# Kernel optimization log

Hardware: AMD Instinct MI355X
Metric: run time of the kernel (lower is better)

## Reference

```python
import jax, jax.numpy as jnp
import numpy as np

D_MODEL = 1024
N_HEADS = 16
FACTOR = 2
KEY_DIM = D_MODEL // N_HEADS            # 64
HEAD_DIM = D_MODEL * FACTOR // N_HEADS  # 128
SCALING = KEY_DIM ** -0.5
BSZ, SEQ = 2, 2048


def _rel_pos(slen):
    # angle: 1/10000**linspace(0,1,key_dim//2), each value repeated twice
    half = jnp.asarray(1.0) / jnp.power(10000.0, jnp.linspace(0.0, 1.0, KEY_DIM // 2))
    angle = jnp.repeat(half, 2)                              # [key_dim]
    decay = jnp.log(1.0 - 2.0 ** (-5.0 - jnp.arange(N_HEADS, dtype=jnp.float32)))  # [h], negative
    idx = jnp.arange(slen, dtype=jnp.float32)
    sin = jnp.sin(idx[:, None] * angle[None, :])             # [s, key_dim]
    cos = jnp.cos(idx[:, None] * angle[None, :])
    diff = idx[:, None] - idx[None, :]                       # [s, s]
    tril = diff >= 0
    mask = jnp.where(tril[None], jnp.exp(diff[None] * decay[:, None, None]), 0.0)  # [h, s, s]
    mask = mask / jnp.sqrt(mask.sum(axis=-1, keepdims=True))
    return sin, cos, mask


def _rotate_every_two(x):
    x1 = x[..., ::2]
    x2 = x[..., 1::2]
    return jnp.stack((-x2, x1), axis=-1).reshape(x.shape)


def _theta_shift(x, sin, cos):
    return x * cos + _rotate_every_two(x) * sin


def setup_inputs() -> dict:
    key = jax.random.key(0)
    ks = jax.random.split(key, 11)
    s = 1.0 / np.sqrt(D_MODEL)
    s2 = 1.0 / np.sqrt(D_MODEL * FACTOR)
    return {
        "x": jax.random.normal(ks[0], (BSZ, SEQ, D_MODEL), jnp.float32),
        "q_w": jax.random.uniform(ks[1], (D_MODEL, D_MODEL), jnp.float32, -s, s),
        "q_b": jax.random.uniform(ks[2], (D_MODEL,), jnp.float32, -s, s),
        "k_w": jax.random.uniform(ks[3], (D_MODEL, D_MODEL), jnp.float32, -s, s),
        "k_b": jax.random.uniform(ks[4], (D_MODEL,), jnp.float32, -s, s),
        "v_w": jax.random.uniform(ks[5], (D_MODEL, D_MODEL * FACTOR), jnp.float32, -s, s),
        "v_b": jax.random.uniform(ks[6], (D_MODEL * FACTOR,), jnp.float32, -s, s),
        "g_w": jax.random.uniform(ks[7], (D_MODEL, D_MODEL * FACTOR), jnp.float32, -s, s),
        "g_b": jax.random.uniform(ks[8], (D_MODEL * FACTOR,), jnp.float32, -s, s),
        "o_w": jax.random.uniform(ks[9], (D_MODEL * FACTOR, D_MODEL), jnp.float32, -s2, s2),
        "o_b": jax.random.uniform(ks[10], (D_MODEL,), jnp.float32, -s2, s2),
    }


def _forward(x, q_w, q_b, k_w, k_b, v_w, v_b, g_w, g_b, o_w, o_b):
    bsz, slen, _ = x.shape
    sin, cos, mask = _rel_pos(slen)
    q = x @ q_w + q_b
    k = (x @ k_w + k_b) * SCALING
    v = x @ v_w + v_b
    g = x @ g_w + g_b
    # [b, h, s, key_dim]
    q = q.reshape(bsz, slen, N_HEADS, KEY_DIM).transpose(0, 2, 1, 3)
    k = k.reshape(bsz, slen, N_HEADS, KEY_DIM).transpose(0, 2, 1, 3)
    qr = _theta_shift(q, sin, cos)
    kr = _theta_shift(k, sin, cos)
    vr = v.reshape(bsz, slen, N_HEADS, HEAD_DIM).transpose(0, 2, 1, 3)  # [b,h,s,head_dim]
    qk = jnp.einsum('bhmd,bhnd->bhmn', qr, kr) * mask                  # decay-masked scores
    denom = jnp.clip(jnp.abs(jax.lax.stop_gradient(qk).sum(axis=-1, keepdims=True)), 1.0, None)
    qk = qk / denom
    out = jnp.einsum('bhmn,bhnd->bhmd', qk, vr).transpose(0, 2, 1, 3)  # [b,s,h,head_dim]
    # per-head LayerNorm over head_dim, no affine
    mu = out.mean(axis=-1, keepdims=True)
    var = out.var(axis=-1, keepdims=True)
    out = (out - mu) / jnp.sqrt(var + 1e-5)
    out = out.reshape(bsz, slen, N_HEADS * HEAD_DIM)
    out = jax.nn.silu(g) * out
    return out @ o_w + o_b


def reference(x, q_w, q_b, k_w, k_b, v_w, v_b, g_w, g_b, o_w, o_b):
    return _forward(x, q_w, q_b, k_w, k_b, v_w, v_b, g_w, g_b, o_w, o_b)
```

## Files before the change

### kernel.cpp

```cpp
#include <hip/hip_runtime.h>
#include <hip/hip_bf16.h>


typedef __hip_bfloat16 bf16;
typedef short bf16x4 __attribute__((ext_vector_type(4)));
typedef short bf16x8 __attribute__((ext_vector_type(8)));
typedef float floatx4 __attribute__((ext_vector_type(4)));

#define B_SZ 2
#define SEQ 2048
#define NH 16
#define KD 64
#define HD 128

#define ASYNC16(gp, lp)                                                             \
  __builtin_amdgcn_global_load_lds(                                                 \
      (const __attribute__((address_space(1))) unsigned int*)(unsigned long long)(const void*)(gp), \
      (__attribute__((address_space(3))) unsigned int*)(unsigned int)(unsigned long long)(void*)(lp), \
      16, 0, 0)

__device__ __forceinline__ float b2f(bf16 x) { return __bfloat162float(x); }
__device__ __forceinline__ bf16 f2b(float x) { return __float2bfloat16(x); }

#define MFMA16(a, bb, c) __builtin_amdgcn_mfma_f32_16x16x32_bf16(a, bb, c, 0, 0, 0)

__global__ void convert_k(const float* __restrict__ in, bf16* __restrict__ out) {
  int i = blockIdx.x * 256 + threadIdx.x;
  float4 v = reinterpret_cast<const float4*>(in)[i];
  union { bf16 h[4]; bf16x4 v4; } u;
  u.h[0] = f2b(v.x); u.h[1] = f2b(v.y); u.h[2] = f2b(v.z); u.h[3] = f2b(v.w);
  reinterpret_cast<bf16x4*>(out)[i] = u.v4;
}

__global__ void transpose_k(const float* __restrict__ in, bf16* __restrict__ out,
                            int K, int N) {
  __shared__ float tile[32][33];
  int tx = threadIdx.x, ty = threadIdx.y;
  int n0 = blockIdx.x * 32, k0 = blockIdx.y * 32;
#pragma unroll
  for (int j = 0; j < 4; ++j)
    tile[ty + j * 8][tx] = in[(size_t)(k0 + ty + j * 8) * N + n0 + tx];
  __syncthreads();
#pragma unroll
  for (int j = 0; j < 4; ++j)
    out[(size_t)(n0 + ty + j * 8) * K + k0 + tx] = f2b(tile[tx][ty + j * 8]);
}

template <int BM, int BN, int KDIM, int MODE>
__global__ __launch_bounds__(256, 2) void gemm_bt(
    const bf16* __restrict__ A, const bf16* __restrict__ Bt, int Ndim,
    const float* __restrict__ bias_q, const float* __restrict__ bias_k,
    const float* __restrict__ bias_v, const float* __restrict__ bias_g,
    float* __restrict__ outCqk, bf16* __restrict__ out_v,
    float* __restrict__ out_g, float* __restrict__ outF) {
  __shared__ bf16 As[BM * 32];
  __shared__ bf16 Bs[BN * 32];
  const int tid = threadIdx.x;
  const int wave = tid >> 6, lane = tid & 63;
  const int quad = lane >> 4, l16 = lane & 15;
  const int m0 = blockIdx.y * BM, n0 = blockIdx.x * BN;
  constexpr int FI = BM / 32;
  constexpr int FJ = BN / 32;
  const int wm = (wave >> 1) * (BM / 2), wn = (wave & 1) * (BN / 2);

  floatx4 acc[FI][FJ] = {};

  for (int k0 = 0; k0 < KDIM; k0 += 32) {
#pragma unroll
    for (int j = 0; j < BM / 64; ++j) {
      int cbase = (j * 4 + wave) * 64;
      int c = cbase + lane;
      const bf16* g = A + (size_t)(m0 + (c >> 2)) * KDIM + k0 + (c & 3) * 8;
      ASYNC16(g, &As[cbase * 8]);
    }
#pragma unroll
    for (int j = 0; j < BN / 64; ++j) {
      int cbase = (j * 4 + wave) * 64;
      int c = cbase + lane;
      const bf16* g = Bt + (size_t)(n0 + (c >> 2)) * KDIM + k0 + (c & 3) * 8;
      ASYNC16(g, &Bs[cbase * 8]);
    }
    __syncthreads();

    bf16x8 af[FI], bfr[FJ];
#pragma unroll
    for (int i = 0; i < FI; ++i)
      af[i] = *(const bf16x8*)&As[(wm + i * 16 + l16) * 32 + quad * 8];
#pragma unroll
    for (int j = 0; j < FJ; ++j)
      bfr[j] = *(const bf16x8*)&Bs[(wn + j * 16 + l16) * 32 + quad * 8];
#pragma unroll
    for (int i = 0; i < FI; ++i)
#pragma unroll
      for (int j = 0; j < FJ; ++j)
        acc[i][j] = MFMA16(af[i], bfr[j], acc[i][j]);
    __syncthreads();
  }

#pragma unroll
  for (int i = 0; i < FI; ++i) {
#pragma unroll
    for (int j = 0; j < FJ; ++j) {
      int gn = n0 + wn + j * 16 + l16;
      if (MODE == 0 && gn >= 2048 && gn < 4096) {
        int jj = gn - 2048;
        int s0 = m0 + wm + i * 16 + quad * 4;
        union { bf16 e[4]; unsigned long long u8; } pk;
#pragma unroll
        for (int r = 0; r < 4; ++r) pk.e[r] = f2b(acc[i][j][r] + bias_v[jj]);
        int b2 = s0 >> 11, srel = s0 & 2047;
        int h2 = jj >> 7, dloc = jj & 127;
        size_t bh2 = (size_t)b2 * NH + h2;
        size_t idx = ((bh2 * 64 + (srel >> 5)) * 8 + (dloc >> 4)) * 512 +
                     (size_t)(((srel >> 3) & 3) * 16 + (dloc & 15)) * 8 +
                     (srel & 7);
        *(unsigned long long*)&out_v[idx] = pk.u8;
      } else {
#pragma unroll
        for (int r = 0; r < 4; ++r) {
          int gm = m0 + wm + i * 16 + quad * 4 + r;
          float v = acc[i][j][r];
          if (MODE == 1) {
            v += bias_q[gn];
            outF[(size_t)gm * Ndim + gn] = v;
          } else {
            if (gn < 2048) {
              bool is_k = gn >= 1024;
              int jj = is_k ? gn - 1024 : gn;
              v += is_k ? bias_k[jj] : bias_q[jj];
              if (is_k) v *= 0.125f;
              outCqk[(size_t)gm * 2048 + gn] = v;
            } else {
              int jj = gn - 4096;
              v += bias_g[jj];
              out_g[(size_t)gm * 2048 + jj] = v;
            }
          }
        }
      }
    }
  }
}

__global__ void router_k(const float* __restrict__ Cqk,
                         bf16* __restrict__ qh, bf16* __restrict__ ql,
                         bf16* __restrict__ kh, bf16* __restrict__ kl) {
  int t = blockIdx.x * 256 + threadIdx.x;
  int row = t >> 10, pc = t & 1023;
  int b = row >> 11, s = row & 2047;
  bool is_k = pc >= 512;
  int jj = (pc - (is_k ? 512 : 0)) * 2;
  int h = jj >> 6, d = jj & 63, ii = d >> 1;
  float2 v = *(const float2*)&Cqk[(size_t)row * 2048 + pc * 2];
  float half = exp2f(-(float)ii * (13.287712379549449f / 31.0f));
  float ang = (float)s * half;
  float sn = sinf(ang), cs = cosf(ang);
  float e = v.x * cs - v.y * sn;
  float o = v.y * cs + v.x * sn;
  bf16 eh = f2b(e), oh = f2b(o);
  bf16 el = f2b(e - b2f(eh)), ol = f2b(o - b2f(oh));
  size_t idx = (((size_t)b * NH + h) * SEQ + s) * KD + d;
  bf16* ph = is_k ? kh : qh;
  bf16* pl = is_k ? kl : ql;
  union { bf16 h2[2]; unsigned u; } uh, ul;
  uh.h2[0] = eh; uh.h2[1] = oh;
  ul.h2[0] = el; ul.h2[1] = ol;
  *(unsigned*)&ph[idx] = uh.u;
  *(unsigned*)&pl[idx] = ul.u;
}

__global__ __launch_bounds__(256, 4) void retention_k(
    const bf16* __restrict__ qh, const bf16* __restrict__ ql,
    const bf16* __restrict__ kh, const bf16* __restrict__ kl,
    const bf16* __restrict__ vf, const float* __restrict__ g,
    bf16* __restrict__ gated) {
  __shared__ bf16 KHs[2][32 * 64];
  __shared__ bf16 KLs[2][32 * 64];
  const int tid = threadIdx.x;
  const int wave = tid >> 6, lane = tid & 63;
  const int quad = lane >> 4, l16 = lane & 15;
  const int bid = blockIdx.x;
  const int grp_raw = bid & 31;
  const int bh = bid >> 5;
  const int h = bh & 15, b = bh >> 4;
  const int grp = ((bh >> 3) & 1) ? (31 - grp_raw) : grp_raw;
  const int st = grp * 4 + wave;
  const int m0 = st * 16;
  const int ntiles = 2 * grp + 2;

  const float t = exp2f(-(float)(5 + h));
  const float lng = log1pf(-t);
  const float log2g = lng * 1.44269504088896340736f;

  float rf;
  {
    int m = m0 + l16;
    rf = exp2f((float)m * log2g) *
         rsqrtf(-expm1f((float)(m + 1) * lng) / t);
  }
  const float gstep = exp2f(-32.0f * log2g);
  float cfq[8];
#pragma unroll
  for (int i = 0; i < 8; ++i) {
    int hh = i >> 2, r = i & 3;
    cfq[i] = exp2f(-(float)(hh * 16 + quad * 4 + r) * log2g);
  }

  const size_t qoff = ((size_t)bh * SEQ + m0 + l16) * KD;
  bf16x8 aq0h = *(const bf16x8*)&qh[qoff + quad * 8];
  bf16x8 aq1h = *(const bf16x8*)&qh[qoff + 32 + quad * 8];
  bf16x8 aq0l = *(const bf16x8*)&ql[qoff + quad * 8];
  bf16x8 aq1l = *(const bf16x8*)&ql[qoff + 32 + quad * 8];

  floatx4 oacc[8] = {};
  float rs = 0.f;

  const bf16* khb = kh + (size_t)bh * SEQ * KD;
  const bf16* klb = kl + (size_t)bh * SEQ * KD;
  const bf16* vfb = vf + (size_t)bh * 64 * 8 * 512;
  const int lo8 = lane * 8;

  auto stage = [&](int nt, int buf) {
    const int n0s = nt * 32;
#pragma unroll
    for (int j = 0; j < 2; ++j) {
      int cc = wave * 2 + j;
      const bf16* src = (cc < 4) ? khb : klb;
      bf16* dst = (cc < 4) ? KHs[buf] : KLs[buf];
      int r = ((cc & 3) * 8) + (lane >> 3);
      int s = lane & 7;
      int q = (s - r) & 7;
      ASYNC16(src + (size_t)(n0s + r) * KD + q * 8, &dst[(cc & 3) * 512]);
    }
  };

  auto buildPA = [&](const floatx4* sc, int n0) -> bf16x8 {
    const int m = m0 + l16;
    const bool full = (m0 >= n0 + 31);
    unsigned d[4];
#pragma unroll
    for (int hh = 0; hh < 2; ++hh) {
      float p[4];
#pragma unroll
      for (int r = 0; r < 4; ++r) {
        float pv;
        if (full) {
          pv = sc[hh][r] * rf * cfq[hh * 4 + r];
        } else {
          int n = n0 + hh * 16 + quad * 4 + r;
          pv = (m >= n) ? sc[hh][r] * rf * cfq[hh * 4 + r] : 0.f;
        }
        rs += pv;
        p[r] = pv;
      }
      union { bf16 hx[2]; unsigned u; } u0, u1;
      u0.hx[0] = f2b(p[0]); u0.hx[1] = f2b(p[1]);
      u1.hx[0] = f2b(p[2]); u1.hx[1] = f2b(p[3]);
      d[hh * 2 + 0] = u0.u;
      d[hh * 2 + 1] = u1.u;
    }
    unsigned a0 = d[0], b0 = d[2];
    asm("v_permlane32_swap_b32 %0, %1" : "+v"(a0), "+v"(b0));
    asm("v_permlane16_swap_b32 %0, %1" : "+v"(a0), "+v"(b0));
    unsigned a1 = d[1], b1 = d[3];
    asm("v_permlane32_swap_b32 %0, %1" : "+v"(a1), "+v"(b1));
    asm("v_permlane16_swap_b32 %0, %1" : "+v"(a1), "+v"(b1));
    union { unsigned u[4]; bf16x8 v; } pu;
    pu.u[0] = a0; pu.u[1] = a1; pu.u[2] = b0; pu.u[3] = b1;
    return pu.v;
  };

  stage(0, 0);
  for (int nt = 0; nt < ntiles; ++nt) {
    const int n0 = nt * 32;
    const int cur = nt & 1;
    asm volatile("s_waitcnt vmcnt(0) lgkmcnt(0)" ::: "memory");
    __syncthreads();

    const bool act = (n0 <= m0 + 15);

    bf16x8 vv[8];
    if (act) {
#pragma unroll
      for (int c = 0; c < 8; ++c)
        vv[c] = *(const bf16x8*)(vfb + ((size_t)nt * 8 + c) * 512 + lo8);
    }

    {
      int pf = (nt + 1 < ntiles) ? nt + 1 : nt;
      stage(pf, cur ^ 1);
    }

    if (act) {
      floatx4 sc[2];
#pragma unroll
      for (int hh = 0; hh < 2; ++hh) {
        int krow = hh * 16 + l16;
        int c0 = ((quad + krow) & 7) * 8;
        int c1 = ((quad + 4 + krow) & 7) * 8;
        bf16x8 bkh0 = *(const bf16x8*)&KHs[cur][krow * 64 + c0];
        bf16x8 bkh1 = *(const bf16x8*)&KHs[cur][krow * 64 + c1];
        bf16x8 bkl0 = *(const bf16x8*)&KLs[cur][krow * 64 + c0];
        bf16x8 bkl1 = *(const bf16x8*)&KLs[cur][krow * 64 + c1];
        floatx4 z1 = {0.f, 0.f, 0.f, 0.f}, z2 = z1, z3 = z1;
        z1 = MFMA16(bkh0, aq0h, z1);
        z2 = MFMA16(bkh0, aq0l, z2);
        z3 = MFMA16(bkl0, aq0h, z3);
        z1 = MFMA16(bkh1, aq1h, z1);
        z2 = MFMA16(bkh1, aq1l, z2);
        z3 = MFMA16(bkl1, aq1h, z3);
        sc[hh] = z1 + z2 + z3;
      }

      bf16x8 pa = buildPA(sc, n0);
      rf *= gstep;

#pragma unroll
      for (int dt = 0; dt < 8; ++dt)
        oacc[dt] = MFMA16(pa, vv[dt], oacc[dt]);
    }
  }

  {
    float v = rs;
    v += __shfl_xor(v, 16);
    v += __shfl_xor(v, 32);
    float inv_den[4];
#pragma unroll
    for (int r = 0; r < 4; ++r) {
      float dsum = __shfl(v, quad * 4 + r);
      inv_den[r] = 1.0f / fmaxf(fabsf(dsum), 1.0f);
    }
    float s1[4] = {}, s2[4] = {};
#pragma unroll
    for (int dt = 0; dt < 8; ++dt) {
#pragma unroll
      for (int r = 0; r < 4; ++r) {
        float vv2 = oacc[dt][r] * inv_den[r];
        oacc[dt][r] = vv2;
        s1[r] += vv2;
        s2[r] += vv2 * vv2;
      }
    }
    float mean[4], istd[4];
#pragma unroll
    for (int r = 0; r < 4; ++r) {
      float a = s1[r], q2 = s2[r];
      a += __shfl_xor(a, 1); a += __shfl_xor(a, 2);
      a += __shfl_xor(a, 4); a += __shfl_xor(a, 8);
      q2 += __shfl_xor(q2, 1); q2 += __shfl_xor(q2, 2);
      q2 += __shfl_xor(q2, 4); q2 += __shfl_xor(q2, 8);
      mean[r] = a * (1.0f / 128.0f);
      float var = q2 * (1.0f / 128.0f) - mean[r] * mean[r];
      istd[r] = rsqrtf(fmaxf(var, 0.0f) + 1e-5f);
    }
#pragma unroll
    for (int dt = 0; dt < 8; ++dt) {
#pragma unroll
      for (int r = 0; r < 4; ++r) {
        int m = m0 + quad * 4 + r;
        int col = h * HD + dt * 16 + l16;
        float vv2 = (oacc[dt][r] - mean[r]) * istd[r];
        float gv = g[((size_t)b * SEQ + m) * 2048 + col];
        float sg = gv / (1.0f + expf(-gv));
        gated[((size_t)b * SEQ + m) * 2048 + col] = f2b(sg * vv2);
      }
    }
  }
}

extern "C" void kernel_launch(void* const* d_in, const int* in_sizes, int n_in,
                              void* d_out, int out_size, void* d_ws,
                              size_t ws_size, hipStream_t stream) {
  const float* x   = (const float*)d_in[0];
  const float* q_w = (const float*)d_in[1];
  const float* q_b = (const float*)d_in[2];
  const float* k_w = (const float*)d_in[3];
  const float* k_b = (const float*)d_in[4];
  const float* v_w = (const float*)d_in[5];
  const float* v_b = (const float*)d_in[6];
  const float* g_w = (const float*)d_in[7];
  const float* g_b = (const float*)d_in[8];
  const float* o_w = (const float*)d_in[9];
  const float* o_b = (const float*)d_in[10];

  char* ws = (char*)d_ws;
  bf16* Wt    = (bf16*)ws; ws += (size_t)6144 * 1024 * 2;
  bf16* oT    = (bf16*)ws; ws += (size_t)1024 * 2048 * 2;
  bf16* xb    = (bf16*)ws; ws += (size_t)4096 * 1024 * 2;
  float* Cqk  = (float*)ws; ws += (size_t)4096 * 2048 * 4;
  bf16* qhb   = (bf16*)ws; ws += (size_t)32 * 2048 * 64 * 2;
  bf16* qlb   = (bf16*)ws; ws += (size_t)32 * 2048 * 64 * 2;
  bf16* khb   = (bf16*)ws; ws += (size_t)32 * 2048 * 64 * 2;
  bf16* klb   = (bf16*)ws; ws += (size_t)32 * 2048 * 64 * 2;
  bf16* vfb   = (bf16*)ws; ws += (size_t)32 * 64 * 8 * 512 * 2;
  float* gbuf = (float*)ws; ws += (size_t)2 * 2048 * 2048 * 4;
  bf16* gated = (bf16*)ws; ws += (size_t)4096 * 2048 * 2;

  convert_k<<<(4096 * 1024 / 4) / 256, 256, 0, stream>>>(x, xb);

  dim3 tb(32, 8);
  transpose_k<<<dim3(1024 / 32, 1024 / 32), tb, 0, stream>>>(q_w, Wt, 1024, 1024);
  transpose_k<<<dim3(1024 / 32, 1024 / 32), tb, 0, stream>>>(k_w, Wt + (size_t)1024 * 1024, 1024, 1024);
  transpose_k<<<dim3(2048 / 32, 1024 / 32), tb, 0, stream>>>(v_w, Wt + (size_t)2048 * 1024, 1024, 2048);
  transpose_k<<<dim3(2048 / 32, 1024 / 32), tb, 0, stream>>>(g_w, Wt + (size_t)4096 * 1024, 1024, 2048);
  transpose_k<<<dim3(1024 / 32, 2048 / 32), tb, 0, stream>>>(o_w, oT, 2048, 1024);

  gemm_bt<128, 128, 1024, 0><<<dim3(6144 / 128, 4096 / 128), 256, 0, stream>>>(
      xb, Wt, 6144, q_b, k_b, v_b, g_b, Cqk, vfb, gbuf, nullptr);

  router_k<<<(4096 * 1024) / 256, 256, 0, stream>>>(Cqk, qhb, qlb, khb, klb);

  retention_k<<<dim3(1024), 256, 0, stream>>>(
      qhb, qlb, khb, klb, vfb, gbuf, gated);

  gemm_bt<128, 64, 2048, 1><<<dim3(1024 / 64, 4096 / 128), 256, 0, stream>>>(
      gated, oT, 1024, o_b, nullptr, nullptr, nullptr, nullptr, nullptr,
      nullptr, (float*)d_out);
}
```

Before: 337.1 us.

## Fuse rotary theta-shift and hi/lo bf16 split into QKV GEMM epilogue

The separate router kernel is removed. The QKV projection GEMM epilogue now applies the bias, the K scaling, the rotary sin/cos rotation (taking the pair partner via a lane shuffle) and the hi/lo bf16 split, then writes q/k straight to the head-major buffers. This drops the large fp32 Cqk intermediate write and re-read and one kernel launch. In exchange the GEMM epilogue does per-element transcendental math and narrow 2-byte scattered stores, which may lengthen the epilogue and raise register pressure.

```diff
diff --git a/kernel.cpp b/kernel.cpp
--- a/kernel.cpp
+++ b/kernel.cpp
@@ -51,8 +51,10 @@
     const bf16* __restrict__ A, const bf16* __restrict__ Bt, int Ndim,
     const float* __restrict__ bias_q, const float* __restrict__ bias_k,
     const float* __restrict__ bias_v, const float* __restrict__ bias_g,
-    float* __restrict__ outCqk, bf16* __restrict__ out_v,
-    float* __restrict__ out_g, float* __restrict__ outF) {
+    bf16* __restrict__ qh, bf16* __restrict__ ql,
+    bf16* __restrict__ kh, bf16* __restrict__ kl,
+    bf16* __restrict__ out_v, float* __restrict__ out_g,
+    float* __restrict__ outF) {
   __shared__ bf16 As[BM * 32];
   __shared__ bf16 Bs[BN * 32];
   const int tid = threadIdx.x;
@@ -102,7 +104,32 @@
 #pragma unroll
     for (int j = 0; j < FJ; ++j) {
       int gn = n0 + wn + j * 16 + l16;
-      if (MODE == 0 && gn >= 2048 && gn < 4096) {
+      if (MODE == 0 && gn < 2048) {
+        bool is_k = gn >= 1024;
+        int jq = is_k ? gn - 1024 : gn;
+        int hd = jq >> 6, d = jq & 63;
+        float halfv = exp2f(-(float)(d >> 1) * (13.287712379549449f / 31.0f));
+        bf16* ph = is_k ? kh : qh;
+        bf16* pl = is_k ? kl : ql;
+        float bias = is_k ? bias_k[jq] : bias_q[jq];
+#pragma unroll
+        for (int r = 0; r < 4; ++r) {
+          int gm = m0 + wm + i * 16 + quad * 4 + r;
+          float v = acc[i][j][r] + bias;
+          if (is_k) v *= 0.125f;
+          int srel = gm & 2047, b2 = gm >> 11;
+          float ang = (float)srel * halfv;
+          float sn = sinf(ang), cs = cosf(ang);
+          float partner = __shfl_xor(v, 1);
+          float res = (gn & 1) ? (v * cs + partner * sn)
+                               : (v * cs - partner * sn);
+          bf16 rh = f2b(res);
+          bf16 rl = f2b(res - b2f(rh));
+          size_t idx = (((size_t)b2 * NH + hd) * SEQ + srel) * KD + d;
+          ph[idx] = rh;
+          pl[idx] = rl;
+        }
+      } else if (MODE == 0 && gn >= 2048 && gn < 4096) {
         int jj = gn - 2048;
         int s0 = m0 + wm + i * 16 + quad * 4;
         union { bf16 e[4]; unsigned long long u8; } pk;
@@ -124,49 +151,14 @@
             v += bias_q[gn];
             outF[(size_t)gm * Ndim + gn] = v;
           } else {
-            if (gn < 2048) {
-              bool is_k = gn >= 1024;
-              int jj = is_k ? gn - 1024 : gn;
-              v += is_k ? bias_k[jj] : bias_q[jj];
-              if (is_k) v *= 0.125f;
-              outCqk[(size_t)gm * 2048 + gn] = v;
-            } else {
-              int jj = gn - 4096;
-              v += bias_g[jj];
-              out_g[(size_t)gm * 2048 + jj] = v;
-            }
+            int jj = gn - 4096;
+            v += bias_g[jj];
+            out_g[(size_t)gm * 2048 + jj] = v;
           }
         }
       }
     }
   }
-}
-
-__global__ void router_k(const float* __restrict__ Cqk,
-                         bf16* __restrict__ qh, bf16* __restrict__ ql,
-                         bf16* __restrict__ kh, bf16* __restrict__ kl) {
-  int t = blockIdx.x * 256 + threadIdx.x;
-  int row = t >> 10, pc = t & 1023;
-  int b = row >> 11, s = row & 2047;
-  bool is_k = pc >= 512;
-  int jj = (pc - (is_k ? 512 : 0)) * 2;
-  int h = jj >> 6, d = jj & 63, ii = d >> 1;
-  float2 v = *(const float2*)&Cqk[(size_t)row * 2048 + pc * 2];
-  float half = exp2f(-(float)ii * (13.287712379549449f / 31.0f));
-  float ang = (float)s * half;
-  float sn = sinf(ang), cs = cosf(ang);
-  float e = v.x * cs - v.y * sn;
-  float o = v.y * cs + v.x * sn;
-  bf16 eh = f2b(e), oh = f2b(o);
-  bf16 el = f2b(e - b2f(eh)), ol = f2b(o - b2f(oh));
-  size_t idx = (((size_t)b * NH + h) * SEQ + s) * KD + d;
-  bf16* ph = is_k ? kh : qh;
-  bf16* pl = is_k ? kl : ql;
-  union { bf16 h2[2]; unsigned u; } uh, ul;
-  uh.h2[0] = eh; uh.h2[1] = oh;
-  ul.h2[0] = el; ul.h2[1] = ol;
-  *(unsigned*)&ph[idx] = uh.u;
-  *(unsigned*)&pl[idx] = ul.u;
 }
 
 __global__ __launch_bounds__(256, 4) void retention_k(
@@ -388,7 +380,6 @@
   bf16* Wt    = (bf16*)ws; ws += (size_t)6144 * 1024 * 2;
   bf16* oT    = (bf16*)ws; ws += (size_t)1024 * 2048 * 2;
   bf16* xb    = (bf16*)ws; ws += (size_t)4096 * 1024 * 2;
-  float* Cqk  = (float*)ws; ws += (size_t)4096 * 2048 * 4;
   bf16* qhb   = (bf16*)ws; ws += (size_t)32 * 2048 * 64 * 2;
   bf16* qlb   = (bf16*)ws; ws += (size_t)32 * 2048 * 64 * 2;
   bf16* khb   = (bf16*)ws; ws += (size_t)32 * 2048 * 64 * 2;
@@ -407,14 +398,13 @@
   transpose_k<<<dim3(1024 / 32, 2048 / 32), tb, 0, stream>>>(o_w, oT, 2048, 1024);
 
   gemm_bt<128, 128, 1024, 0><<<dim3(6144 / 128, 4096 / 128), 256, 0, stream>>>(
-      xb, Wt, 6144, q_b, k_b, v_b, g_b, Cqk, vfb, gbuf, nullptr);
-
-  router_k<<<(4096 * 1024) / 256, 256, 0, stream>>>(Cqk, qhb, qlb, khb, klb);
+      xb, Wt, 6144, q_b, k_b, v_b, g_b, qhb, qlb, khb, klb, vfb, gbuf,
+      nullptr);
 
   retention_k<<<dim3(1024), 256, 0, stream>>>(
       qhb, qlb, khb, klb, vfb, gbuf, gated);
 
   gemm_bt<128, 64, 2048, 1><<<dim3(1024 / 64, 4096 / 128), 256, 0, stream>>>(
       gated, oT, 1024, o_b, nullptr, nullptr, nullptr, nullptr, nullptr,
-      nullptr, (float*)d_out);
+      nullptr, nullptr, nullptr, nullptr, (float*)d_out);
 }
```

Measured after the change: 1.142 ms. 239% more time.
